# Performance work log

Hardware: AMD Instinct MI355X
Metric: run time of the kernel (lower is better)

## Reference

```python
import jax, jax.numpy as jnp
import numpy as np

EPS = 1e-6
NUM_HEADS = 2
DIM = 64
DIM_OUT = 128
SR = 4
SAMPLE_NUM = 784


def layer_norm(x, g, b, eps=1e-5):
    m = jnp.mean(x, -1, keepdims=True)
    v = jnp.mean((x - m) ** 2, -1, keepdims=True)
    return (x - m) * jax.lax.rsqrt(v + eps) * g + b


def gaussian_filt(x, kernel_size, sigma):
    # depthwise gaussian blur, x: [B, Ch, H, W]
    ch = x.shape[1]
    coord = jnp.arange(kernel_size, dtype=x.dtype)
    xg, yg = jnp.meshgrid(coord, coord, indexing='xy')
    mean = (kernel_size - 1) / 2.0
    var = sigma ** 2.0
    gk = jnp.exp(-((xg - mean) ** 2 + (yg - mean) ** 2) / (2.0 * var)) / (2.0 * np.pi * var)
    gk = gk / jnp.sum(gk)
    kernel = jnp.broadcast_to(gk[None, None], (ch, 1, kernel_size, kernel_size))
    pad = (kernel_size - 1) // 2
    return jax.lax.conv_general_dilated(
        x, kernel, (1, 1), [(pad, pad), (pad, pad)],
        dimension_numbers=('NCHW', 'OIHW', 'NCHW'), feature_group_count=ch)


def reconstruct_feature(feature, mask, kernel_size, sigma):
    if kernel_size <= 1:
        return feature
    feature = feature * mask
    out = gaussian_filt(jnp.concatenate([feature, mask], axis=1), kernel_size, sigma)
    fi = out[:, :-1]
    mi = out[:, -1:]
    fi = fi / (mi + EPS)
    fi = fi * (mi > 0).astype(feature.dtype)
    return feature + (1 - mask) * fi


def token2map(x, loc, H, W, kernel_size, sigma):
    # scatter tokens onto an HxW grid by rounded location, then gaussian-fill holes
    B, N, C = x.shape
    loc = jnp.clip(loc, 0, 1) * jnp.array([W - 1, H - 1], dtype=loc.dtype)
    loc = jnp.round(loc).astype(jnp.int32)
    idx = loc[..., 0] + loc[..., 1] * W + jnp.arange(B, dtype=jnp.int32)[:, None] * (H * W)
    src = jnp.concatenate([x, jnp.ones((B, N, 1), x.dtype)], axis=-1).reshape(B * N, C + 1)
    out = jax.ops.segment_sum(src, idx.reshape(-1), num_segments=B * H * W)
    out = out.reshape(B, H, W, C + 1).transpose(0, 3, 1, 2)
    feat, mask = out[:, :-1], out[:, -1:]
    feat = feat / (mask + EPS)
    mask = (mask > 0).astype(feat.dtype)
    feat = feat * mask
    return reconstruct_feature(feat, mask, kernel_size, sigma)


def grid_sample_bilinear(img, gx, gy):
    # F.grid_sample: bilinear, zeros padding, align_corners=False
    # img: [B, C, H, W]; gx, gy in [-1, 1]: [B, N]
    B, C, H, W = img.shape
    ix = ((gx + 1) * W - 1) / 2
    iy = ((gy + 1) * H - 1) / 2
    x0 = jnp.floor(ix)
    y0 = jnp.floor(iy)
    wx1 = ix - x0
    wy1 = iy - y0
    imgf = img.reshape(B, C, H * W)

    def corner(xc, yc, w):
        valid = (xc >= 0) & (xc < W) & (yc >= 0) & (yc < H)
        xi = jnp.clip(xc, 0, W - 1).astype(jnp.int32)
        yi = jnp.clip(yc, 0, H - 1).astype(jnp.int32)
        lin = (yi * W + xi)[:, None, :]                      # [B,1,N]
        v = jnp.take_along_axis(imgf, lin, axis=2)           # [B,C,N]
        return v * (w * valid)[:, None, :]

    out = (corner(x0, y0, (1 - wx1) * (1 - wy1))
           + corner(x0 + 1, y0, wx1 * (1 - wy1))
           + corner(x0, y0 + 1, (1 - wx1) * wy1)
           + corner(x0 + 1, y0 + 1, wx1 * wy1))
    return out.transpose(0, 2, 1)                            # [B,N,C]


def _forward(x, pos, pos_embed, noise_u, norm_g, norm_b, conf_w, conf_b,
             norm1_g, norm1_b, q_w, k_w, v_w, proj_w, proj_b, sr_w, sr_b,
             srnorm_g, srnorm_b, fc_w, fc_b, norm2_g, norm2_b,
             fc1_w, fc1_b, fc2_w, fc2_b, H, W, N_grid):
    B, N, C = x.shape
    # --- DownLayer: confidence + gumbel top-k over adaptive tokens ---
    conf = layer_norm(x, norm_g, norm_b) @ conf_w + conf_b            # [B,N,1]
    noise = -jnp.log(-jnp.log(noise_u + EPS) + EPS)                   # gumbel noise
    scores = (conf[:, N_grid:] + noise)[..., 0]                       # [B,N-N_grid]
    _, idx = jax.lax.top_k(scores, SAMPLE_NUM)                        # [B,k]
    x_down = jnp.concatenate(
        [x[:, :N_grid], jnp.take_along_axis(x[:, N_grid:], idx[:, :, None], axis=1)], axis=1)
    pos_down = jnp.concatenate(
        [pos[:, :N_grid], jnp.take_along_axis(pos[:, N_grid:], idx[:, :, None], axis=1)], axis=1)

    # --- MyBlock: fc(x) + sr-attention, then MLP (eval mode: dropouts off) ---
    Nd = x_down.shape[1]
    xn = layer_norm(x_down, norm1_g, norm1_b)
    xsn = layer_norm(x, norm1_g, norm1_b)
    q = xn @ q_w                                                      # [B,Nd,DIM_OUT]
    fmap = token2map(xsn, pos, H, W, SR - 1, 2.0)                     # [B,C,H,W]
    xs = jax.lax.conv_general_dilated(
        fmap, sr_w, (SR, SR), 'VALID',
        dimension_numbers=('NCHW', 'OIHW', 'NCHW')) + sr_b[None, :, None, None]
    xs = xs.reshape(B, C, -1).transpose(0, 2, 1)                      # [B,Ns,C]
    xs = layer_norm(xs, srnorm_g, srnorm_b)
    k = xs @ k_w
    v = xs @ v_w
    hd = DIM_OUT // NUM_HEADS
    qh = q.reshape(B, Nd, NUM_HEADS, hd).transpose(0, 2, 1, 3)
    kh = k.reshape(B, -1, NUM_HEADS, hd).transpose(0, 2, 1, 3)
    vh = v.reshape(B, -1, NUM_HEADS, hd).transpose(0, 2, 1, 3)
    scale = (DIM // NUM_HEADS) ** -0.5                                # head_dim from input dim per source
    attn = jax.nn.softmax(jnp.einsum('bhqd,bhkd->bhqk', qh, kh) * scale, axis=-1)
    o = jnp.einsum('bhqk,bhkd->bhqd', attn, vh).transpose(0, 2, 1, 3).reshape(B, Nd, DIM_OUT)
    o = o @ proj_w + proj_b
    x2 = x_down @ fc_w + fc_b + o                                     # use_fc branch (dim_out != dim), alpha=1
    xn2 = layer_norm(x2, norm2_g, norm2_b)
    x2 = x2 + (jax.nn.gelu(xn2 @ fc1_w + fc1_b, approximate=False) @ fc2_w + fc2_b)

    # --- get_pos_embed: bilinear grid_sample of pos_embed at pos_down ---
    Cp = pos_embed.shape[-1]
    pe = jnp.broadcast_to(pos_embed.reshape(1, H, W, Cp).transpose(0, 3, 1, 2), (B, Cp, H, W))
    g = pos_down * 2 - 1
    pos_feat = grid_sample_bilinear(pe, g[..., 0], g[..., 1])         # [B,Nd,Cp]
    return x2 + pos_feat


def setup_inputs() -> dict:
    key = jax.random.key(0)
    ks = jax.random.split(key, 16)
    B, N = 64, 3136
    N_grid = 49

    def w(k, shape, fan):
        return jax.random.normal(k, shape, jnp.float32) / np.sqrt(fan)

    d = {}
    d['x'] = jax.random.normal(ks[0], (B, N, DIM), jnp.float32)
    d['pos'] = jax.random.uniform(ks[1], (B, N, 2), jnp.float32)
    d['pos_embed'] = jax.random.normal(ks[2], (1, N, DIM_OUT), jnp.float32) * 0.02
    d['noise_u'] = jax.random.uniform(ks[3], (B, N - N_grid, 1), jnp.float32)
    d['norm_g'] = jnp.ones(DIM); d['norm_b'] = jnp.zeros(DIM)
    d['conf_w'] = w(ks[4], (DIM, 1), DIM); d['conf_b'] = jnp.zeros(1)
    d['norm1_g'] = jnp.ones(DIM); d['norm1_b'] = jnp.zeros(DIM)
    d['q_w'] = w(ks[5], (DIM, DIM_OUT), DIM)
    d['k_w'] = w(ks[6], (DIM, DIM_OUT), DIM)
    d['v_w'] = w(ks[7], (DIM, DIM_OUT), DIM)
    d['proj_w'] = w(ks[8], (DIM_OUT, DIM_OUT), DIM_OUT); d['proj_b'] = jnp.zeros(DIM_OUT)
    d['sr_w'] = w(ks[9], (DIM, DIM, SR, SR), DIM * SR * SR); d['sr_b'] = jnp.zeros(DIM)
    d['srnorm_g'] = jnp.ones(DIM); d['srnorm_b'] = jnp.zeros(DIM)
    d['fc_w'] = w(ks[10], (DIM, DIM_OUT), DIM); d['fc_b'] = jnp.zeros(DIM_OUT)
    d['norm2_g'] = jnp.ones(DIM_OUT); d['norm2_b'] = jnp.zeros(DIM_OUT)
    d['fc1_w'] = w(ks[11], (DIM_OUT, 4 * DIM_OUT), DIM_OUT); d['fc1_b'] = jnp.zeros(4 * DIM_OUT)
    d['fc2_w'] = w(ks[12], (4 * DIM_OUT, DIM_OUT), 4 * DIM_OUT); d['fc2_b'] = jnp.zeros(DIM_OUT)
    d['H'] = 56; d['W'] = 56; d['N_grid'] = N_grid
    return d


def reference(x, pos, pos_embed, noise_u, norm_g, norm_b, conf_w, conf_b,
              norm1_g, norm1_b, q_w, k_w, v_w, proj_w, proj_b, sr_w, sr_b,
              srnorm_g, srnorm_b, fc_w, fc_b, norm2_g, norm2_b,
              fc1_w, fc1_b, fc2_w, fc2_b, H, W, N_grid):
    return _forward(x, pos, pos_embed, noise_u, norm_g, norm_b, conf_w, conf_b,
                    norm1_g, norm1_b, q_w, k_w, v_w, proj_w, proj_b, sr_w, sr_b,
                    srnorm_g, srnorm_b, fc_w, fc_b, norm2_g, norm2_b,
                    fc1_w, fc1_b, fc2_w, fc2_b, H, W, N_grid)
```

## Files before the change

kernel.cpp:

```cpp
#include <hip/hip_runtime.h>
#include <math.h>

#define DEVINL __device__ __forceinline__

constexpr int B_ = 64;
constexpr int N_ = 3136;
constexpr int C_ = 64;
constexpr int NG = 49;
constexpr int NSAMP = 784;
constexpr int ND = NG + NSAMP;
constexpr int NREST = N_ - NG;
constexpr int H_ = 56, W_ = 56;
constexpr int HW = H_ * W_;
constexpr int BHW = B_ * HW;
constexpr int NS = 14 * 14;
constexpr int KPAD = 224;
constexpr float LN_EPS = 1e-5f;
constexpr float EPS6 = 1e-6f;

typedef __attribute__((ext_vector_type(8))) short short8;
typedef __attribute__((ext_vector_type(4))) float f32x4;

DEVINL unsigned short f2bf(float f) {
  unsigned int u = __float_as_uint(f);
  unsigned int r = u + 0x7FFFu + ((u >> 16) & 1u);
  return (unsigned short)(r >> 16);
}

DEVINL float gelu_fast(float v) {
  float x = v * 0.70710678118654752f;
  float ax = fabsf(x);
  float t = 1.f / fmaf(0.3275911f, ax, 1.f);
  float poly = t * fmaf(t, fmaf(t, fmaf(t, fmaf(t, 1.061405429f, -1.453152027f),
                        1.421413741f), -0.284496736f), 0.254829592f);
  float e = 1.f - poly * __expf(-x * x);
  float erfv = copysignf(e, x);
  return 0.5f * v * (1.f + erfv);
}

__global__ __launch_bounds__(256) void k_conf(
    const float* __restrict__ x, const float* __restrict__ ng, const float* __restrict__ nb,
    const float* __restrict__ cw, const float* __restrict__ cb,
    const float* __restrict__ nu, double* __restrict__ scores) {
  int t = blockIdx.x * 256 + threadIdx.x;
  if (t >= B_ * N_) return;
  int b = t / N_, n = t - b * N_;
  if (n < NG) return;
  const float4* row = (const float4*)(x + (size_t)t * C_);
  float v[C_];
#pragma unroll
  for (int i = 0; i < 16; ++i) {
    float4 r = row[i];
    v[4*i] = r.x; v[4*i+1] = r.y; v[4*i+2] = r.z; v[4*i+3] = r.w;
  }
  double sd = 0.0;
#pragma unroll
  for (int i = 0; i < C_; ++i) sd += (double)v[i];
  double md = sd * (1.0/64.0);
  double vd = 0.0;
#pragma unroll
  for (int i = 0; i < C_; ++i) { double d = (double)v[i] - md; vd += d * d; }
  vd *= (1.0/64.0);
  double rsd = 1.0 / sqrt(vd + 1e-5);
  double conf = (double)cb[0];
#pragma unroll
  for (int i = 0; i < C_; ++i) {
    double xnv = ((double)v[i] - md) * rsd;
    conf += (xnv * (double)ng[i] + (double)nb[i]) * (double)cw[i];
  }
  double u = (double)nu[(size_t)b * NREST + (n - NG)];
  double noise = -log(-log(u + 1e-6) + 1e-6);
  scores[(size_t)b * NREST + (n - NG)] = conf + noise;
}

constexpr int NB = 2048;

__global__ __launch_bounds__(256) void k_topk2(const double* __restrict__ scores,
                                               int* __restrict__ idx) {
  __shared__ double sk[NREST];
  __shared__ int hist[NB];
  __shared__ int bstart[NB];
  __shared__ int fill[NB];
  __shared__ unsigned short order[NREST];
  __shared__ float redmin[256], redmax[256];
  __shared__ int scanbuf[256];
  int b = blockIdx.x, tid = threadIdx.x;
  const double* sc = scores + (size_t)b * NREST;
  float lmin = 3.4e38f, lmax = -3.4e38f;
  for (int i = tid; i < NREST; i += 256) {
    double d = sc[i];
    sk[i] = d;
    float f = (float)d;
    lmin = fminf(lmin, f); lmax = fmaxf(lmax, f);
  }
  for (int i = tid; i < NB; i += 256) hist[i] = 0;
  redmin[tid] = lmin; redmax[tid] = lmax;
  __syncthreads();
  for (int s = 128; s > 0; s >>= 1) {
    if (tid < s) {
      redmin[tid] = fminf(redmin[tid], redmin[tid + s]);
      redmax[tid] = fmaxf(redmax[tid], redmax[tid + s]);
    }
    __syncthreads();
  }
  float fmn = redmin[0];
  float scale = (float)NB / fmaxf(redmax[0] - fmn, 1e-30f);
  for (int i = tid; i < NREST; i += 256) {
    float f = (float)sk[i];
    int bn = (int)((f - fmn) * scale);
    bn = bn < 0 ? 0 : (bn > NB - 1 ? NB - 1 : bn);
    atomicAdd(&hist[bn], 1);
  }
  __syncthreads();
  int base = tid * 8;
  int s_t = 0;
#pragma unroll
  for (int i = 0; i < 8; ++i) s_t += hist[base + i];
  scanbuf[tid] = s_t;
  __syncthreads();
  int val = s_t;
  for (int off = 1; off < 256; off <<= 1) {
    int other = (tid + off < 256) ? scanbuf[tid + off] : 0;
    __syncthreads();
    val += other;
    scanbuf[tid] = val;
    __syncthreads();
  }
  int run = val - s_t;
#pragma unroll
  for (int i = 7; i >= 0; --i) {
    bstart[base + i] = run;
    run += hist[base + i];
  }
  __syncthreads();
  for (int i = tid; i < NB; i += 256) fill[i] = bstart[i];
  __syncthreads();
  for (int i = tid; i < NREST; i += 256) {
    float f = (float)sk[i];
    int bn = (int)((f - fmn) * scale);
    bn = bn < 0 ? 0 : (bn > NB - 1 ? NB - 1 : bn);
    int pos = atomicAdd(&fill[bn], 1);
    order[pos] = (unsigned short)i;
  }
  __syncthreads();
  for (int i = tid; i < NREST; i += 256) {
    double ke = sk[i];
    float f = (float)ke;
    int bn = (int)((f - fmn) * scale);
    bn = bn < 0 ? 0 : (bn > NB - 1 ? NB - 1 : bn);
    int st = bstart[bn], m = hist[bn];
    int r = st;
    for (int p = st; p < st + m; ++p) {
      int j = order[p];
      double kj = sk[j];
      r += (int)((kj > ke) | ((kj == ke) & (j < i)));
    }
    if (r < NSAMP) idx[(size_t)b * NSAMP + r] = i;
  }
}

__global__ __launch_bounds__(256) void k_gather_ln(
    const float* __restrict__ x, const float* __restrict__ pos, const int* __restrict__ idx,
    const float* __restrict__ n1g, const float* __restrict__ n1b,
    float* __restrict__ xd, float* __restrict__ xn, float* __restrict__ pd) {
  int t = blockIdx.x * 256 + threadIdx.x;
  if (t >= B_ * ND) return;
  int b = t / ND, r = t - b * ND;
  int srcn = (r < NG) ? r : (NG + idx[(size_t)b * NSAMP + (r - NG)]);
  const float4* row = (const float4*)(x + ((size_t)b * N_ + srcn) * C_);
  float4* xdr = (float4*)(xd + (size_t)t * C_);
  float v[C_];
  float s = 0.f, ss = 0.f;
#pragma unroll
  for (int i = 0; i < 16; ++i) {
    float4 rr = row[i];
    xdr[i] = rr;
    v[4*i] = rr.x; v[4*i+1] = rr.y; v[4*i+2] = rr.z; v[4*i+3] = rr.w;
    s += rr.x + rr.y + rr.z + rr.w;
    ss += rr.x*rr.x + rr.y*rr.y + rr.z*rr.z + rr.w*rr.w;
  }
  float m = s * (1.f/64.f);
  float var = ss * (1.f/64.f) - m*m;
  float rs = rsqrtf(var + LN_EPS);
#pragma unroll
  for (int i = 0; i < C_; ++i)
    xn[(size_t)t * C_ + i] = (v[i] - m) * rs * n1g[i] + n1b[i];
  pd[(size_t)2*t]   = pos[((size_t)b * N_ + srcn) * 2];
  pd[(size_t)2*t+1] = pos[((size_t)b * N_ + srcn) * 2 + 1];
}

__global__ __launch_bounds__(256) void k_link(
    const float* __restrict__ pos, int* __restrict__ head, int* __restrict__ next) {
  int tok = blockIdx.x * 256 + threadIdx.x;
  if (tok >= B_ * N_) return;
  int b = tok / N_;
  double px = fmin(fmax((double)pos[(size_t)2*tok],   0.0), 1.0) * (double)(W_ - 1);
  double py = fmin(fmax((double)pos[(size_t)2*tok+1], 0.0), 1.0) * (double)(H_ - 1);
  int xi = (int)rint(px), yi = (int)rint(py);
  int p = b * HW + yi * W_ + xi;
  next[tok] = atomicExch(&head[p], tok);
}

__global__ __launch_bounds__(256) void k_accum(
    const float* __restrict__ x, const float* __restrict__ n1g, const float* __restrict__ n1b,
    const int* __restrict__ head, const int* __restrict__ next, float* __restrict__ S) {
  int gt = blockIdx.x * 256 + threadIdx.x;
  int p = gt >> 6, lane = gt & 63;
  if (p >= B_ * HW) return;
  float g = n1g[lane], bb = n1b[lane];
  float acc = 0.f, cnt = 0.f;
  int tok = head[p];
  while (tok >= 0) {
    float v = x[(size_t)tok * C_ + lane];
    float s = v, ss = v * v;
#pragma unroll
    for (int m = 32; m > 0; m >>= 1) {
      s += __shfl_xor(s, m);
      ss += __shfl_xor(ss, m);
    }
    float mean = s * (1.f/64.f);
    float var = ss * (1.f/64.f) - mean * mean;
    float rs = rsqrtf(var + LN_EPS);
    acc += (v - mean) * rs * g + bb;
    cnt += 1.f;
    tok = next[tok];
  }
  float* base = S + (size_t)p * 65;
  base[lane] = acc;
  if (lane == 0) base[64] = cnt;
}

__global__ __launch_bounds__(256) void k_transpose(const float* __restrict__ S,
                                                   float* __restrict__ T,
                                                   float* __restrict__ M) {
  __shared__ float ls[64 * 65];
  int g0 = blockIdx.x * 64;
  int b = g0 / HW, p0 = g0 - b * HW;
  const float4* src = (const float4*)(S + (size_t)g0 * 65);
  for (int i = threadIdx.x; i < (64 * 65) / 4; i += 256)
    *(float4*)&ls[i * 4] = src[i];
  __syncthreads();
  for (int i = threadIdx.x; i < 64 * 64; i += 256) {
    int c = i >> 6, px = i & 63;
    T[((size_t)(b * 64 + c)) * HW + p0 + px] = ls[px * 65 + c];
  }
  for (int i = threadIdx.x; i < 64; i += 256)
    M[(size_t)g0 + i] = ls[i * 65 + 64];
}

__global__ __launch_bounds__(256) void k_coef(const float* __restrict__ M, float* __restrict__ Kc) {
  int t = blockIdx.x * 256 + threadIdx.x;
  if (t >= BHW) return;
  int b = t / HW, p = t - b * HW;
  int y = p / W_, x = p - y * W_;
  const float* Mb = M + (size_t)b * HW;
  const float e1 = 0.882496902584595f;
  const float e2 = 0.778800783071405f;
  const float Z = 1.f + 4.f * (e1 + e2);
  float m0 = Mb[p];
  float mb0 = m0 > 0.f ? 1.f : 0.f;
  float cfac = mb0 / (m0 + EPS6);
  float sc[9];
  float mi = 0.f;
  int q = 0;
#pragma unroll
  for (int dy = -1; dy <= 1; ++dy) {
#pragma unroll
    for (int dx = -1; dx <= 1; ++dx) {
      int ny = y + dy, nx = x + dx;
      bool in = (ny >= 0 && ny < H_ && nx >= 0 && nx < W_);
      float w = ((dx == 0 && dy == 0) ? 1.f : ((dx*dx + dy*dy) == 1 ? e1 : e2)) / Z;
      float mm = in ? Mb[ny * W_ + nx] : 0.f;
      float mb = mm > 0.f ? 1.f : 0.f;
      mi += w * mb;
      sc[q] = in ? (w * mb / (mm + EPS6)) : 0.f;
      ++q;
    }
  }
  float outer = (1.f - mb0) * ((mi > 0.f ? 1.f : 0.f) / (mi + EPS6));
#pragma unroll
  for (int qq = 0; qq < 9; ++qq) {
    float cq = outer * sc[qq];
    if (qq == 4) cq += cfac;
    Kc[(size_t)qq * BHW + t] = cq;
  }
}

__global__ __launch_bounds__(256) void k_filter2(
    const float* __restrict__ T, const float* __restrict__ Kc, float* __restrict__ P) {
  int plane = blockIdx.x;
  int b = plane >> 6, c = plane & 63;
  int tid = threadIdx.x;
  const float* Tp = T + (size_t)plane * HW;
  const float* Kb = Kc + (size_t)b * HW;
  for (int p0 = 0; p0 < HW; p0 += 256) {
    int p = p0 + tid;
    if (p < HW) {
      int y = p / W_, x = p - y * W_;
      float acc = 0.f;
      int q = 0;
#pragma unroll
      for (int dy = -1; dy <= 1; ++dy) {
#pragma unroll
        for (int dx = -1; dx <= 1; ++dx) {
          int ny = y + dy; ny = ny < 0 ? 0 : (ny > H_ - 1 ? H_ - 1 : ny);
          int nx = x + dx; nx = nx < 0 ? 0 : (nx > W_ - 1 ? W_ - 1 : nx);
          acc += Kb[(size_t)q * BHW + p] * Tp[ny * W_ + nx];
          ++q;
        }
      }
      int j = (y >> 2) * 14 + (x >> 2);
      int colb = ((y & 3) << 2) + (x & 3);
      P[((size_t)(b * NS + j)) * 1024 + c * 16 + colb] = acc;
    }
  }
}

__global__ __launch_bounds__(256) void k_wtp(const float* __restrict__ srw,
                                             unsigned short* __restrict__ Wcp) {
  int t = blockIdx.x * 256 + threadIdx.x;
  if (t >= 65536) return;
  int j = t & 7;
  int n = (t >> 3) & 63;
  int s = (t >> 9) & 15;
  int ch = t >> 13;
  int k = ch * 128 + (s >> 2) * 32 + (s & 3) * 8 + j;
  int ci = k >> 4, r = k & 15;
  Wcp[t] = f2bf(srw[(((size_t)n * 64 + ci) << 4) + r]);
}

__global__ __launch_bounds__(256) void k_wpack(const float* __restrict__ W1, const float* __restrict__ W2,
    unsigned short* __restrict__ W1q, unsigned short* __restrict__ W2q) {
  int t = blockIdx.x * 256 + threadIdx.x;
  if (t >= 65536) return;
  {
    int j = t & 7;
    int nl = (t >> 3) & 63;
    int s = (t >> 9) & 15;
    int hh = t >> 13;
    int k = (s >> 2) * 32 + (s & 3) * 8 + j;
    int n = hh * 64 + nl;
    W1q[t] = f2bf(W1[(size_t)k * 512 + n]);
  }
  {
    int j = t & 7;
    int n = (t >> 3) & 127;
    int s = (t >> 10) & 7;
    int hh = t >> 13;
    int k = hh * 64 + (s >> 2) * 32 + (s & 3) * 8 + j;
    W2q[t] = f2bf(W2[(size_t)k * 128 + n]);
  }
}

__global__ __launch_bounds__(256) void k_conv(
    const float* __restrict__ P, const unsigned short* __restrict__ Wcp,
    const float* __restrict__ bias, float* __restrict__ out) {
  __shared__ __align__(16) unsigned short sA[64 * 128];
  __shared__ __align__(16) unsigned short sW[8192];
  int bm = blockIdx.x * 64;
  int tid = threadIdx.x;
  int wv = tid >> 6, lane = tid & 63, quad = lane >> 4, l16 = lane & 15;

  const short8* gw = (const short8*)Wcp;
  short8* dw = (short8*)sW;

  short8 rw[4];
  float4 fa[4][2];
#pragma unroll
  for (int i = 0; i < 4; ++i) rw[i] = gw[i * 256 + tid];
#pragma unroll
  for (int i = 0; i < 4; ++i) {
    int u = i * 256 + tid;
    int row = u >> 4, ck = u & 15;
    const float* src = P + (size_t)(bm + row) * 1024 + ck * 8;
    fa[i][0] = *(const float4*)src;
    fa[i][1] = *(const float4*)(src + 4);
  }

  f32x4 acc[4];
#pragma unroll
  for (int ct = 0; ct < 4; ++ct) acc[ct] = (f32x4){0.f, 0.f, 0.f, 0.f};

  for (int ch = 0; ch < 8; ++ch) {
#pragma unroll
    for (int i = 0; i < 4; ++i) {
      dw[i * 256 + tid] = rw[i];
      int u = i * 256 + tid;
      int row = u >> 4, ck = u & 15;
      short8 p;
      p[0]=(short)f2bf(fa[i][0].x); p[1]=(short)f2bf(fa[i][0].y);
      p[2]=(short)f2bf(fa[i][0].z); p[3]=(short)f2bf(fa[i][0].w);
      p[4]=(short)f2bf(fa[i][1].x); p[5]=(short)f2bf(fa[i][1].y);
      p[6]=(short)f2bf(fa[i][1].z); p[7]=(short)f2bf(fa[i][1].w);
      *(short8*)&sA[row * 128 + (((ck ^ row) & 15) << 3)] = p;
    }
    __syncthreads();
    if (ch < 7) {
      int wbase = (ch + 1) * 1024;
#pragma unroll
      for (int i = 0; i < 4; ++i) rw[i] = gw[wbase + i * 256 + tid];
#pragma unroll
      for (int i = 0; i < 4; ++i) {
        int u = i * 256 + tid;
        int row = u >> 4, ck = u & 15;
        const float* src = P + (size_t)(bm + row) * 1024 + (ch + 1) * 128 + ck * 8;
        fa[i][0] = *(const float4*)src;
        fa[i][1] = *(const float4*)(src + 4);
      }
    }
#pragma unroll
    for (int kc = 0; kc < 4; ++kc) {
      int row = wv * 16 + l16;
      int ck = kc * 4 + quad;
      short8 af = *(const short8*)&sA[row * 128 + (((ck ^ row) & 15) << 3)];
      int s = kc * 4 + quad;
#pragma unroll
      for (int ct = 0; ct < 4; ++ct) {
        short8 bf = *(const short8*)&sW[(s * 64 + ct * 16 + l16) << 3];
        acc[ct] = __builtin_amdgcn_mfma_f32_16x16x32_bf16(af, bf, acc[ct], 0, 0, 0);
      }
    }
    __syncthreads();
  }
#pragma unroll
  for (int ct = 0; ct < 4; ++ct)
#pragma unroll
    for (int r = 0; r < 4; ++r) {
      int row = bm + wv * 16 + quad * 4 + r;
      int col = ct * 16 + l16;
      out[(size_t)row * 64 + col] = acc[ct][r] + bias[col];
    }
}

__global__ __launch_bounds__(256) void k_gemm(
    const float* __restrict__ A, const float* __restrict__ Bw,
    const float* __restrict__ bias, const float* __restrict__ add,
    float* __restrict__ Cout, int M, int N, int K) {
  __shared__ float sA[16][68];
  __shared__ float sB[16][64];
  int bm = blockIdx.x * 64, bn = blockIdx.y * 64;
  int tid = threadIdx.x;
  int tx = tid & 15, ty = tid >> 4;
  float acc[4][4] = {{0.f}};
  for (int k0 = 0; k0 < K; k0 += 16) {
    int e = tid << 2;
    int am = e >> 4, ak = e & 15;
    float4 a4 = *(const float4*)(A + (size_t)(bm + am) * K + k0 + ak);
    sA[ak + 0][am] = a4.x; sA[ak + 1][am] = a4.y; sA[ak + 2][am] = a4.z; sA[ak + 3][am] = a4.w;
    int bk = e >> 6, nn = e & 63;
    float4 b4 = *(const float4*)(Bw + (size_t)(k0 + bk) * N + bn + nn);
    *(float4*)&sB[bk][nn] = b4;
    __syncthreads();
#pragma unroll
    for (int kk = 0; kk < 16; ++kk) {
      float a[4], bb[4];
#pragma unroll
      for (int i = 0; i < 4; ++i) a[i] = sA[kk][ty * 4 + i];
#pragma unroll
      for (int i = 0; i < 4; ++i) bb[i] = sB[kk][tx * 4 + i];
#pragma unroll
      for (int i = 0; i < 4; ++i)
#pragma unroll
        for (int jj = 0; jj < 4; ++jj) acc[i][jj] += a[i] * bb[jj];
    }
    __syncthreads();
  }
#pragma unroll
  for (int i = 0; i < 4; ++i) {
    int row = bm + ty * 4 + i;
#pragma unroll
    for (int jj = 0; jj < 4; ++jj) {
      int col = bn + tx * 4 + jj;
      float v = acc[i][jj];
      if (bias) v += bias[col];
      if (add) v += add[(size_t)row * N + col];
      Cout[(size_t)row * N + col] = v;
    }
  }
}

__global__ __launch_bounds__(256) void k_mlp(
    const float* __restrict__ A, const unsigned short* __restrict__ W1q, const float* __restrict__ b1,
    const unsigned short* __restrict__ W2q, const float* __restrict__ b2, float* __restrict__ out) {
  __shared__ __align__(16) unsigned short sA[64 * 128];
  __shared__ __align__(16) unsigned short sW1[8192];
  __shared__ __align__(16) unsigned short sW2[8192];
  __shared__ __align__(16) unsigned short sH[4][16 * 64];
  int bm = blockIdx.x * 64;
  int tid = threadIdx.x;
  int wv = tid >> 6, lane = tid & 63, quad = lane >> 4, l16 = lane & 15;

  const short8* g1 = (const short8*)W1q;
  const short8* g2 = (const short8*)W2q;
  short8* d1 = (short8*)sW1;
  short8* d2 = (short8*)sW2;

  short8 r1[4], r2[4];
#pragma unroll
  for (int i = 0; i < 4; ++i) {
    r1[i] = g1[i * 256 + tid];
    r2[i] = g2[i * 256 + tid];
  }

  for (int t = tid; t < 64 * 16; t += 256) {
    int row = t >> 4, ck = t & 15;
    const float* src = A + (size_t)(bm + row) * 128 + ck * 8;
    float4 a = *(const float4*)src;
    float4 c = *(const float4*)(src + 4);
    short8 p;
    p[0]=(short)f2bf(a.x); p[1]=(short)f2bf(a.y); p[2]=(short)f2bf(a.z); p[3]=(short)f2bf(a.w);
    p[4]=(short)f2bf(c.x); p[5]=(short)f2bf(c.y); p[6]=(short)f2bf(c.z); p[7]=(short)f2bf(c.w);
    *(short8*)&sA[row * 128 + (((ck ^ row) & 15) << 3)] = p;
  }
  __syncthreads();

  f32x4 oacc[8];
#pragma unroll
  for (int ct = 0; ct < 8; ++ct) oacc[ct] = (f32x4){0.f, 0.f, 0.f, 0.f};

  for (int hh = 0; hh < 8; ++hh) {
#pragma unroll
    for (int i = 0; i < 4; ++i) {
      d1[i * 256 + tid] = r1[i];
      d2[i * 256 + tid] = r2[i];
    }
    __syncthreads();
    if (hh < 7) {
      int base = (hh + 1) * 1024;
#pragma unroll
      for (int i = 0; i < 4; ++i) {
        r1[i] = g1[base + i * 256 + tid];
        r2[i] = g2[base + i * 256 + tid];
      }
    }
    f32x4 acc1[4];
#pragma unroll
    for (int ct = 0; ct < 4; ++ct) acc1[ct] = (f32x4){0.f, 0.f, 0.f, 0.f};
#pragma unroll
    for (int kc = 0; kc < 4; ++kc) {
      int row = wv * 16 + l16;
      int ck = kc * 4 + quad;
      short8 af = *(const short8*)&sA[row * 128 + (((ck ^ row) & 15) << 3)];
      int s = kc * 4 + quad;
#pragma unroll
      for (int ct = 0; ct < 4; ++ct) {
        short8 bf = *(const short8*)&sW1[(s * 64 + ct * 16 + l16) << 3];
        acc1[ct] = __builtin_amdgcn_mfma_f32_16x16x32_bf16(af, bf, acc1[ct], 0, 0, 0);
      }
    }
#pragma unroll
    for (int ct = 0; ct < 4; ++ct)
#pragma unroll
      for (int r = 0; r < 4; ++r) {
        float v = acc1[ct][r] + b1[hh * 64 + ct * 16 + l16];
        v = gelu_fast(v);
        int rit = quad * 4 + r;
        int col = ct * 16 + l16;
        int ck = (col >> 3) ^ (rit & 7);
        sH[wv][rit * 64 + ((ck & 7) << 3) + (col & 7)] = f2bf(v);
      }
#pragma unroll
    for (int kg = 0; kg < 2; ++kg) {
      int ckh = kg * 4 + quad;
      short8 hf = *(const short8*)&sH[wv][l16 * 64 + (((ckh ^ (l16 & 7)) & 7) << 3)];
      int s = kg * 4 + quad;
#pragma unroll
      for (int ct = 0; ct < 8; ++ct) {
        short8 bf = *(const short8*)&sW2[(s * 128 + ct * 16 + l16) << 3];
        oacc[ct] = __builtin_amdgcn_mfma_f32_16x16x32_bf16(hf, bf, oacc[ct], 0, 0, 0);
      }
    }
    __syncthreads();
  }
#pragma unroll
  for (int ct = 0; ct < 8; ++ct)
#pragma unroll
    for (int r = 0; r < 4; ++r) {
      int row = bm + wv * 16 + quad * 4 + r;
      int col = ct * 16 + l16;
      out[(size_t)row * 128 + col] += oacc[ct][r] + b2[col];
    }
}

__global__ __launch_bounds__(256) void k_ln128(const float* __restrict__ in, const float* __restrict__ g,
    const float* __restrict__ bb, float* __restrict__ out, int rows) {
  int t = blockIdx.x * 256 + threadIdx.x;
  if (t >= rows) return;
  const float4* row = (const float4*)(in + (size_t)t * 128);
  float4 v[32];
  float s = 0.f, ss = 0.f;
#pragma unroll
  for (int i = 0; i < 32; ++i) {
    float4 r = row[i]; v[i] = r;
    s += r.x + r.y + r.z + r.w;
    ss += r.x*r.x + r.y*r.y + r.z*r.z + r.w*r.w;
  }
  float m = s * (1.f/128.f);
  float var = ss * (1.f/128.f) - m*m;
  float rs = rsqrtf(var + LN_EPS);
  float4* orow = (float4*)(out + (size_t)t * 128);
#pragma unroll
  for (int i = 0; i < 32; ++i) {
    float4 r = v[i];
    float4 o;
    o.x = (r.x - m) * rs * g[4*i+0] + bb[4*i+0];
    o.y = (r.y - m) * rs * g[4*i+1] + bb[4*i+1];
    o.z = (r.z - m) * rs * g[4*i+2] + bb[4*i+2];
    o.w = (r.w - m) * rs * g[4*i+3] + bb[4*i+3];
    orow[i] = o;
  }
}

__global__ __launch_bounds__(256) void k_ln64(const float* __restrict__ in, const float* __restrict__ g,
    const float* __restrict__ bb, float* __restrict__ out, int rows) {
  int t = blockIdx.x * 256 + threadIdx.x;
  if (t >= rows) return;
  const float4* row = (const float4*)(in + (size_t)t * 64);
  float v[64];
  float s = 0.f, ss = 0.f;
#pragma unroll
  for (int i = 0; i < 16; ++i) {
    float4 r = row[i];
    v[4*i] = r.x; v[4*i+1] = r.y; v[4*i+2] = r.z; v[4*i+3] = r.w;
    s += r.x + r.y + r.z + r.w;
    ss += r.x*r.x + r.y*r.y + r.z*r.z + r.w*r.w;
  }
  float m = s * (1.f/64.f);
  float var = ss * (1.f/64.f) - m*m;
  float rs = rsqrtf(var + LN_EPS);
#pragma unroll
  for (int i = 0; i < 64; ++i)
    out[(size_t)t * 64 + i] = (v[i] - m) * rs * g[i] + bb[i];
}

__global__ __launch_bounds__(256) void k_attn(const float* __restrict__ q,
    const float* __restrict__ kg, const float* __restrict__ vg, float* __restrict__ o) {
  __shared__ __align__(16) unsigned short ldsKP[14848];
  __shared__ __align__(16) unsigned short ldsV[16128];
  int blk = blockIdx.x;
  int chunk = blk % 14;
  int bh = blk / 14;
  int h = bh & 1, b = bh >> 1;
  int tid = threadIdx.x;
  int wv = tid >> 6, lane = tid & 63;
  int quad = lane >> 4, l16 = lane & 15;

  const float* kb = kg + (size_t)b * NS * 128 + h * 64;
  const float* vb = vg + (size_t)b * NS * 128 + h * 64;

  for (int t = tid; t < KPAD * 8; t += 256) {
    int key = t >> 3, ck = t & 7;
    short8 pk, pv;
    if (key < NS) {
      const float* ksrc = kb + (size_t)key * 128 + ck * 8;
      const float* vsrc = vb + (size_t)key * 128 + ck * 8;
      float4 a = *(const float4*)ksrc;
      float4 c = *(const float4*)(ksrc + 4);
      pk[0]=(short)f2bf(a.x); pk[1]=(short)f2bf(a.y); pk[2]=(short)f2bf(a.z); pk[3]=(short)f2bf(a.w);
      pk[4]=(short)f2bf(c.x); pk[5]=(short)f2bf(c.y); pk[6]=(short)f2bf(c.z); pk[7]=(short)f2bf(c.w);
      float4 e = *(const float4*)vsrc;
      float4 g = *(const float4*)(vsrc + 4);
      pv[0]=(short)f2bf(e.x); pv[1]=(short)f2bf(e.y); pv[2]=(short)f2bf(e.z); pv[3]=(short)f2bf(e.w);
      pv[4]=(short)f2bf(g.x); pv[5]=(short)f2bf(g.y); pv[6]=(short)f2bf(g.z); pv[7]=(short)f2bf(g.w);
    } else {
      pk = (short8)0; pv = (short8)0;
    }
    *(short8*)&ldsKP[key * 64 + ((ck ^ (key & 7)) << 3)] = pk;
    *(short8*)&ldsV[key * 72 + ck * 8] = pv;
  }

  int qrow = chunk * 64 + wv * 16 + l16;
  int qrowc = qrow < ND ? qrow : ND - 1;
  const float* qsrc = q + ((size_t)b * ND + qrowc) * 128 + h * 64 + quad * 8;
  short8 aq0, aq1;
  {
    float4 a = *(const float4*)qsrc;
    float4 c = *(const float4*)(qsrc + 4);
    aq0[0]=(short)f2bf(a.x); aq0[1]=(short)f2bf(a.y); aq0[2]=(short)f2bf(a.z); aq0[3]=(short)f2bf(a.w);
    aq0[4]=(short)f2bf(c.x); aq0[5]=(short)f2bf(c.y); aq0[6]=(short)f2bf(c.z); aq0[7]=(short)f2bf(c.w);
    float4 e = *(const float4*)(qsrc + 32);
    float4 g = *(const float4*)(qsrc + 36);
    aq1[0]=(short)f2bf(e.x); aq1[1]=(short)f2bf(e.y); aq1[2]=(short)f2bf(e.z); aq1[3]=(short)f2bf(e.w);
    aq1[4]=(short)f2bf(g.x); aq1[5]=(short)f2bf(g.y); aq1[6]=(short)f2bf(g.z); aq1[7]=(short)f2bf(g.w);
  }
  __syncthreads();

  f32x4 acc[14];
#pragma unroll
  for (int ct = 0; ct < 14; ++ct) {
    int key = ct * 16 + l16;
    short8 bk0 = *(const short8*)&ldsKP[key * 64 + ((quad ^ (key & 7)) << 3)];
    short8 bk1 = *(const short8*)&ldsKP[key * 64 + (((4 + quad) ^ (key & 7)) << 3)];
    f32x4 z = {0.f, 0.f, 0.f, 0.f};
    z = __builtin_amdgcn_mfma_f32_16x16x32_bf16(aq0, bk0, z, 0, 0, 0);
    z = __builtin_amdgcn_mfma_f32_16x16x32_bf16(aq1, bk1, z, 0, 0, 0);
    acc[ct] = z;
  }

  const float scale = 0.17677669529663687f;
  float rmax[4] = {-1e30f, -1e30f, -1e30f, -1e30f};
#pragma unroll
  for (int ct = 0; ct < 14; ++ct) {
    bool msk = (ct * 16 + l16) >= NS;
#pragma unroll
    for (int r = 0; r < 4; ++r) {
      float sv = msk ? -1e30f : acc[ct][r] * scale;
      acc[ct][r] = sv;
      rmax[r] = fmaxf(rmax[r], sv);
    }
  }
#pragma unroll
  for (int m = 1; m < 16; m <<= 1)
#pragma unroll
    for (int r = 0; r < 4; ++r) rmax[r] = fmaxf(rmax[r], __shfl_xor(rmax[r], m));
  float rsum[4] = {0.f, 0.f, 0.f, 0.f};
#pragma unroll
  for (int ct = 0; ct < 14; ++ct)
#pragma unroll
    for (int r = 0; r < 4; ++r) {
      float e = __expf(acc[ct][r] - rmax[r]);
      acc[ct][r] = e;
      rsum[r] += e;
    }
#pragma unroll
  for (int m = 1; m < 16; m <<= 1)
#pragma unroll
    for (int r = 0; r < 4; ++r) rsum[r] += __shfl_xor(rsum[r], m);
  float rinv[4];
#pragma unroll
  for (int r = 0; r < 4; ++r) rinv[r] = 1.f / rsum[r];

  __syncthreads();

#pragma unroll
  for (int ct = 0; ct < 14; ++ct)
#pragma unroll
    for (int r = 0; r < 4; ++r) {
      int prow = wv * 16 + quad * 4 + r;
      ldsKP[prow * 232 + ct * 16 + l16] = f2bf(acc[ct][r] * rinv[r]);
    }
  __syncthreads();

  f32x4 oacc[4];
#pragma unroll
  for (int ot = 0; ot < 4; ++ot) oacc[ot] = (f32x4){0.f, 0.f, 0.f, 0.f};
#pragma unroll
  for (int kc = 0; kc < 7; ++kc) {
    short8 ap = *(const short8*)&ldsKP[(wv * 16 + l16) * 232 + kc * 32 + quad * 8];
    int keybase = kc * 32 + quad * 8;
#pragma unroll
    for (int ot = 0; ot < 4; ++ot) {
      int dcol = ot * 16 + l16;
      short8 bv;
#pragma unroll
      for (int j = 0; j < 8; ++j) bv[j] = (short)ldsV[(keybase + j) * 72 + dcol];
      oacc[ot] = __builtin_amdgcn_mfma_f32_16x16x32_bf16(ap, bv, oacc[ot], 0, 0, 0);
    }
  }

#pragma unroll
  for (int ot = 0; ot < 4; ++ot)
#pragma unroll
    for (int r = 0; r < 4; ++r) {
      int rowg = chunk * 64 + wv * 16 + quad * 4 + r;
      if (rowg < ND)
        o[((size_t)b * ND + rowg) * 128 + h * 64 + ot * 16 + l16] = oacc[ot][r];
    }
}

__global__ __launch_bounds__(256) void k_posfeat(const float* __restrict__ pd,
    const float* __restrict__ pe, float* __restrict__ out) {
  int t = blockIdx.x * 256 + threadIdx.x;
  int row = t >> 5, lane = t & 31;
  if (row >= B_ * ND) return;
  float gx = pd[(size_t)2*row] * 2.f - 1.f;
  float gy = pd[(size_t)2*row+1] * 2.f - 1.f;
  float ix = ((gx + 1.f) * 56.f - 1.f) * 0.5f;
  float iy = ((gy + 1.f) * 56.f - 1.f) * 0.5f;
  float x0 = floorf(ix), y0 = floorf(iy);
  float wx1 = ix - x0, wy1 = iy - y0;
  float wx0 = 1.f - wx1, wy0 = 1.f - wy1;
  float4 acc = make_float4(0.f, 0.f, 0.f, 0.f);
#pragma unroll
  for (int cy = 0; cy < 2; ++cy) {
#pragma unroll
    for (int cx = 0; cx < 2; ++cx) {
      float xc = x0 + (float)cx, yc = y0 + (float)cy;
      float wgt = (cx ? wx1 : wx0) * (cy ? wy1 : wy0);
      bool valid = (xc >= 0.f) && (xc < 56.f) && (yc >= 0.f) && (yc < 56.f);
      if (valid) {
        int lin = (int)yc * 56 + (int)xc;
        float4 pv = ((const float4*)(pe + (size_t)lin * 128))[lane];
        acc.x += wgt * pv.x; acc.y += wgt * pv.y;
        acc.z += wgt * pv.z; acc.w += wgt * pv.w;
      }
    }
  }
  float4* op = (float4*)(out + (size_t)row * 128) + lane;
  float4 cur = *op;
  cur.x += acc.x; cur.y += acc.y; cur.z += acc.z; cur.w += acc.w;
  *op = cur;
}

extern "C" void kernel_launch(void* const* d_in, const int* in_sizes, int n_in,
                              void* d_out, int out_size, void* d_ws, size_t ws_size,
                              hipStream_t stream) {
  const float* x      = (const float*)d_in[0];
  const float* pos    = (const float*)d_in[1];
  const float* pe     = (const float*)d_in[2];
  const float* nu     = (const float*)d_in[3];
  const float* norm_g = (const float*)d_in[4];
  const float* norm_b = (const float*)d_in[5];
  const float* conf_w = (const float*)d_in[6];
  const float* conf_b = (const float*)d_in[7];
  const float* n1g    = (const float*)d_in[8];
  const float* n1b    = (const float*)d_in[9];
  const float* q_w    = (const float*)d_in[10];
  const float* k_w    = (const float*)d_in[11];
  const float* v_w    = (const float*)d_in[12];
  const float* proj_w = (const float*)d_in[13];
  const float* proj_b = (const float*)d_in[14];
  const float* sr_w   = (const float*)d_in[15];
  const float* sr_b   = (const float*)d_in[16];
  const float* srn_g  = (const float*)d_in[17];
  const float* srn_b  = (const float*)d_in[18];
  const float* fc_w   = (const float*)d_in[19];
  const float* fc_b   = (const float*)d_in[20];
  const float* n2g    = (const float*)d_in[21];
  const float* n2b    = (const float*)d_in[22];
  const float* fc1_w  = (const float*)d_in[23];
  const float* fc1_b  = (const float*)d_in[24];
  const float* fc2_w  = (const float*)d_in[25];
  const float* fc2_b  = (const float*)d_in[26];

  char* ws = (char*)d_ws;
  double*         scores = (double*)(ws + 0);
  int*            idx    = (int*)(ws + 1605632);
  float*          xd     = (float*)(ws + 1835008);
  float*          xn     = (float*)(ws + 15728640);
  float*          pd     = (float*)(ws + 29491200);
  float*          qb     = (float*)(ws + 30408704);
  float*          ob     = (float*)(ws + 58720256);
  unsigned short* Wcp    = (unsigned short*)(ws + 86507520);
  unsigned short* W1p    = (unsigned short*)(ws + 86769664);
  unsigned short* W2p    = (unsigned short*)(ws + 86900736);
  char*           big    = ws + 87031808;
  float*          S      = (float*)big;
  float*          T      = qb;
  float*          Kc     = (float*)(big + 52183040);
  float*          P      = (float*)big;
  float*          xs_c   = (float*)(big + 59408384);
  float*          xs_n   = (float*)(big + 62619648);
  float*          kbuf   = (float*)(big + 65830912);
  float*          vbuf   = (float*)(big + 72253440);
  float*          Mbuf   = (float*)(big + 78675968);
  int*            head   = (int*)(big + 79478784);
  int*            nxt    = (int*)(big + 80281600);
  float*          O2     = qb;
  float*          xn2    = ob;
  float*          out    = (float*)d_out;

  k_conf<<<(B_ * N_) / 256, 256, 0, stream>>>(x, norm_g, norm_b, conf_w, conf_b, nu, scores);
  k_topk2<<<B_, 256, 0, stream>>>(scores, idx);
  k_gather_ln<<<(B_ * ND + 255) / 256, 256, 0, stream>>>(x, pos, idx, n1g, n1b, xd, xn, pd);
  hipMemsetAsync(head, 0xFF, (size_t)B_ * HW * sizeof(int), stream);
  k_link<<<(B_ * N_ + 255) / 256, 256, 0, stream>>>(pos, head, nxt);
  k_accum<<<(B_ * HW * 64) / 256, 256, 0, stream>>>(x, n1g, n1b, head, nxt, S);
  k_transpose<<<BHW / 64, 256, 0, stream>>>(S, T, Mbuf);
  k_coef<<<BHW / 256, 256, 0, stream>>>(Mbuf, Kc);
  k_filter2<<<B_ * 64, 256, 0, stream>>>(T, Kc, P);
  k_wtp<<<65536 / 256, 256, 0, stream>>>(sr_w, Wcp);
  k_wpack<<<65536 / 256, 256, 0, stream>>>(fc1_w, fc2_w, W1p, W2p);
  k_conv<<<B_ * NS / 64, 256, 0, stream>>>(P, Wcp, sr_b, xs_c);
  k_ln64<<<(B_ * NS + 255) / 256, 256, 0, stream>>>(xs_c, srn_g, srn_b, xs_n, B_ * NS);
  dim3 g_kv(B_ * NS / 64, 2);
  k_gemm<<<g_kv, 256, 0, stream>>>(xs_n, k_w, nullptr, nullptr, kbuf, B_ * NS, 128, 64);
  k_gemm<<<g_kv, 256, 0, stream>>>(xs_n, v_w, nullptr, nullptr, vbuf, B_ * NS, 128, 64);
  dim3 g_row(B_ * ND / 64, 2);
  k_gemm<<<g_row, 256, 0, stream>>>(xn, q_w, nullptr, nullptr, qb, B_ * ND, 128, 64);
  k_attn<<<B_ * 2 * 14, 256, 0, stream>>>(qb, kbuf, vbuf, ob);
  k_gemm<<<g_row, 256, 0, stream>>>(ob, proj_w, proj_b, nullptr, O2, B_ * ND, 128, 128);
  k_gemm<<<g_row, 256, 0, stream>>>(xd, fc_w, fc_b, O2, out, B_ * ND, 128, 64);
  k_ln128<<<(B_ * ND + 255) / 256, 256, 0, stream>>>(out, n2g, n2b, xn2, B_ * ND);
  k_mlp<<<B_ * ND / 64, 256, 0, stream>>>(xn2, W1p, fc1_b, W2p, fc2_b, out);
  k_posfeat<<<(B_ * ND * 32) / 256, 256, 0, stream>>>(pd, pe, out);
}
```

Measured before the change: 575.1 us.

## Fuse layernorms into conv and MLP GEMM kernels

The separate k_ln64 and k_ln128 kernels are removed. The sr-norm layernorm now runs in the k_conv epilogue, using wave shuffles to reduce each row across its 64 output columns. The norm2 layernorm now runs in the k_mlp prologue, with each lane holding its row's A fragments in registers instead of staging them through LDS. This saves two launches and a full write and re-read of the intermediate activations, at the cost of more registers per thread and a one-pass variance formula.

```diff
diff --git a/kernel.cpp b/kernel.cpp
--- a/kernel.cpp
+++ b/kernel.cpp
@@ -354,7 +354,8 @@
 
 __global__ __launch_bounds__(256) void k_conv(
     const float* __restrict__ P, const unsigned short* __restrict__ Wcp,
-    const float* __restrict__ bias, float* __restrict__ out) {
+    const float* __restrict__ bias, const float* __restrict__ sg,
+    const float* __restrict__ sb, float* __restrict__ xsn) {
   __shared__ __align__(16) unsigned short sA[64 * 128];
   __shared__ __align__(16) unsigned short sW[8192];
   int bm = blockIdx.x * 64;
@@ -422,13 +423,40 @@
     }
     __syncthreads();
   }
+  float vv[4][4];
+  float rsum[4], rss[4];
+#pragma unroll
+  for (int r = 0; r < 4; ++r) { rsum[r] = 0.f; rss[r] = 0.f; }
+#pragma unroll
+  for (int ct = 0; ct < 4; ++ct)
+#pragma unroll
+    for (int r = 0; r < 4; ++r) {
+      float v = acc[ct][r] + bias[ct * 16 + l16];
+      vv[ct][r] = v;
+      rsum[r] += v;
+      rss[r] += v * v;
+    }
+#pragma unroll
+  for (int m = 1; m < 16; m <<= 1)
+#pragma unroll
+    for (int r = 0; r < 4; ++r) {
+      rsum[r] += __shfl_xor(rsum[r], m);
+      rss[r]  += __shfl_xor(rss[r], m);
+    }
+  float mean[4], rsl[4];
+#pragma unroll
+  for (int r = 0; r < 4; ++r) {
+    mean[r] = rsum[r] * (1.f/64.f);
+    float var = rss[r] * (1.f/64.f) - mean[r] * mean[r];
+    rsl[r] = rsqrtf(var + LN_EPS);
+  }
 #pragma unroll
   for (int ct = 0; ct < 4; ++ct)
 #pragma unroll
     for (int r = 0; r < 4; ++r) {
       int row = bm + wv * 16 + quad * 4 + r;
       int col = ct * 16 + l16;
-      out[(size_t)row * 64 + col] = acc[ct][r] + bias[col];
+      xsn[(size_t)row * 64 + col] = (vv[ct][r] - mean[r]) * rsl[r] * sg[col] + sb[col];
     }
 }
 
@@ -480,9 +508,10 @@
 }
 
 __global__ __launch_bounds__(256) void k_mlp(
-    const float* __restrict__ A, const unsigned short* __restrict__ W1q, const float* __restrict__ b1,
-    const unsigned short* __restrict__ W2q, const float* __restrict__ b2, float* __restrict__ out) {
-  __shared__ __align__(16) unsigned short sA[64 * 128];
+    const float* __restrict__ A, const float* __restrict__ gg, const float* __restrict__ gb,
+    const unsigned short* __restrict__ W1q, const float* __restrict__ b1,
+    const unsigned short* __restrict__ W2q, const float* __restrict__ b2,
+    float* __restrict__ out) {
   __shared__ __align__(16) unsigned short sW1[8192];
   __shared__ __align__(16) unsigned short sW2[8192];
   __shared__ __align__(16) unsigned short sH[4][16 * 64];
@@ -502,17 +531,41 @@
     r2[i] = g2[i * 256 + tid];
   }
 
-  for (int t = tid; t < 64 * 16; t += 256) {
-    int row = t >> 4, ck = t & 15;
-    const float* src = A + (size_t)(bm + row) * 128 + ck * 8;
-    float4 a = *(const float4*)src;
-    float4 c = *(const float4*)(src + 4);
-    short8 p;
-    p[0]=(short)f2bf(a.x); p[1]=(short)f2bf(a.y); p[2]=(short)f2bf(a.z); p[3]=(short)f2bf(a.w);
-    p[4]=(short)f2bf(c.x); p[5]=(short)f2bf(c.y); p[6]=(short)f2bf(c.z); p[7]=(short)f2bf(c.w);
-    *(short8*)&sA[row * 128 + (((ck ^ row) & 15) << 3)] = p;
-  }
-  __syncthreads();
+  int row = bm + wv * 16 + l16;
+  const float* arow = A + (size_t)row * 128 + quad * 8;
+  float av[4][8];
+  float s = 0.f, ss = 0.f;
+#pragma unroll
+  for (int kc = 0; kc < 4; ++kc) {
+    float4 a = *(const float4*)(arow + kc * 32);
+    float4 c = *(const float4*)(arow + kc * 32 + 4);
+    av[kc][0]=a.x; av[kc][1]=a.y; av[kc][2]=a.z; av[kc][3]=a.w;
+    av[kc][4]=c.x; av[kc][5]=c.y; av[kc][6]=c.z; av[kc][7]=c.w;
+    s += a.x+a.y+a.z+a.w + c.x+c.y+c.z+c.w;
+    ss += a.x*a.x+a.y*a.y+a.z*a.z+a.w*a.w + c.x*c.x+c.y*c.y+c.z*c.z+c.w*c.w;
+  }
+  s += __shfl_xor(s, 16);  ss += __shfl_xor(ss, 16);
+  s += __shfl_xor(s, 32);  ss += __shfl_xor(ss, 32);
+  float m = s * (1.f/128.f);
+  float var = ss * (1.f/128.f) - m * m;
+  float rs = rsqrtf(var + LN_EPS);
+  short8 af[4];
+#pragma unroll
+  for (int kc = 0; kc < 4; ++kc) {
+    int c0 = kc * 32 + quad * 8;
+    float4 ga = *(const float4*)(gg + c0);
+    float4 gc = *(const float4*)(gg + c0 + 4);
+    float4 ba = *(const float4*)(gb + c0);
+    float4 bc = *(const float4*)(gb + c0 + 4);
+    af[kc][0] = (short)f2bf((av[kc][0]-m)*rs*ga.x + ba.x);
+    af[kc][1] = (short)f2bf((av[kc][1]-m)*rs*ga.y + ba.y);
+    af[kc][2] = (short)f2bf((av[kc][2]-m)*rs*ga.z + ba.z);
+    af[kc][3] = (short)f2bf((av[kc][3]-m)*rs*ga.w + ba.w);
+    af[kc][4] = (short)f2bf((av[kc][4]-m)*rs*gc.x + bc.x);
+    af[kc][5] = (short)f2bf((av[kc][5]-m)*rs*gc.y + bc.y);
+    af[kc][6] = (short)f2bf((av[kc][6]-m)*rs*gc.z + bc.z);
+    af[kc][7] = (short)f2bf((av[kc][7]-m)*rs*gc.w + bc.w);
+  }
 
   f32x4 oacc[8];
 #pragma unroll
@@ -538,14 +591,11 @@
     for (int ct = 0; ct < 4; ++ct) acc1[ct] = (f32x4){0.f, 0.f, 0.f, 0.f};
 #pragma unroll
     for (int kc = 0; kc < 4; ++kc) {
-      int row = wv * 16 + l16;
-      int ck = kc * 4 + quad;
-      short8 af = *(const short8*)&sA[row * 128 + (((ck ^ row) & 15) << 3)];
-      int s = kc * 4 + quad;
+      int sidx = kc * 4 + quad;
 #pragma unroll
       for (int ct = 0; ct < 4; ++ct) {
-        short8 bf = *(const short8*)&sW1[(s * 64 + ct * 16 + l16) << 3];
-        acc1[ct] = __builtin_amdgcn_mfma_f32_16x16x32_bf16(af, bf, acc1[ct], 0, 0, 0);
+        short8 bf = *(const short8*)&sW1[(sidx * 64 + ct * 16 + l16) << 3];
+        acc1[ct] = __builtin_amdgcn_mfma_f32_16x16x32_bf16(af[kc], bf, acc1[ct], 0, 0, 0);
       }
     }
 #pragma unroll
@@ -563,10 +613,10 @@
     for (int kg = 0; kg < 2; ++kg) {
       int ckh = kg * 4 + quad;
       short8 hf = *(const short8*)&sH[wv][l16 * 64 + (((ckh ^ (l16 & 7)) & 7) << 3)];
-      int s = kg * 4 + quad;
+      int sidx = kg * 4 + quad;
 #pragma unroll
       for (int ct = 0; ct < 8; ++ct) {
-        short8 bf = *(const short8*)&sW2[(s * 128 + ct * 16 + l16) << 3];
+        short8 bf = *(const short8*)&sW2[(sidx * 128 + ct * 16 + l16) << 3];
         oacc[ct] = __builtin_amdgcn_mfma_f32_16x16x32_bf16(hf, bf, oacc[ct], 0, 0, 0);
       }
     }
@@ -576,61 +626,10 @@
   for (int ct = 0; ct < 8; ++ct)
 #pragma unroll
     for (int r = 0; r < 4; ++r) {
-      int row = bm + wv * 16 + quad * 4 + r;
+      int orow = bm + wv * 16 + quad * 4 + r;
       int col = ct * 16 + l16;
-      out[(size_t)row * 128 + col] += oacc[ct][r] + b2[col];
-    }
-}
-
-__global__ __launch_bounds__(256) void k_ln128(const float* __restrict__ in, const float* __restrict__ g,
-    const float* __restrict__ bb, float* __restrict__ out, int rows) {
-  int t = blockIdx.x * 256 + threadIdx.x;
-  if (t >= rows) return;
-  const float4* row = (const float4*)(in + (size_t)t * 128);
-  float4 v[32];
-  float s = 0.f, ss = 0.f;
-#pragma unroll
-  for (int i = 0; i < 32; ++i) {
-    float4 r = row[i]; v[i] = r;
-    s += r.x + r.y + r.z + r.w;
-    ss += r.x*r.x + r.y*r.y + r.z*r.z + r.w*r.w;
-  }
-  float m = s * (1.f/128.f);
-  float var = ss * (1.f/128.f) - m*m;
-  float rs = rsqrtf(var + LN_EPS);
-  float4* orow = (float4*)(out + (size_t)t * 128);
-#pragma unroll
-  for (int i = 0; i < 32; ++i) {
-    float4 r = v[i];
-    float4 o;
-    o.x = (r.x - m) * rs * g[4*i+0] + bb[4*i+0];
-    o.y = (r.y - m) * rs * g[4*i+1] + bb[4*i+1];
-    o.z = (r.z - m) * rs * g[4*i+2] + bb[4*i+2];
-    o.w = (r.w - m) * rs * g[4*i+3] + bb[4*i+3];
-    orow[i] = o;
-  }
-}
-
-__global__ __launch_bounds__(256) void k_ln64(const float* __restrict__ in, const float* __restrict__ g,
-    const float* __restrict__ bb, float* __restrict__ out, int rows) {
-  int t = blockIdx.x * 256 + threadIdx.x;
-  if (t >= rows) return;
-  const float4* row = (const float4*)(in + (size_t)t * 64);
-  float v[64];
-  float s = 0.f, ss = 0.f;
-#pragma unroll
-  for (int i = 0; i < 16; ++i) {
-    float4 r = row[i];
-    v[4*i] = r.x; v[4*i+1] = r.y; v[4*i+2] = r.z; v[4*i+3] = r.w;
-    s += r.x + r.y + r.z + r.w;
-    ss += r.x*r.x + r.y*r.y + r.z*r.z + r.w*r.w;
-  }
-  float m = s * (1.f/64.f);
-  float var = ss * (1.f/64.f) - m*m;
-  float rs = rsqrtf(var + LN_EPS);
-#pragma unroll
-  for (int i = 0; i < 64; ++i)
-    out[(size_t)t * 64 + i] = (v[i] - m) * rs * g[i] + bb[i];
+      out[(size_t)orow * 128 + col] += oacc[ct][r] + b2[col];
+    }
 }
 
 __global__ __launch_bounds__(256) void k_attn(const float* __restrict__ q,
@@ -849,7 +848,6 @@
   float*          T      = qb;
   float*          Kc     = (float*)(big + 52183040);
   float*          P      = (float*)big;
-  float*          xs_c   = (float*)(big + 59408384);
   float*          xs_n   = (float*)(big + 62619648);
   float*          kbuf   = (float*)(big + 65830912);
   float*          vbuf   = (float*)(big + 72253440);
@@ -857,7 +855,6 @@
   int*            head   = (int*)(big + 79478784);
   int*            nxt    = (int*)(big + 80281600);
   float*          O2     = qb;
-  float*          xn2    = ob;
   float*          out    = (float*)d_out;
 
   k_conf<<<(B_ * N_) / 256, 256, 0, stream>>>(x, norm_g, norm_b, conf_w, conf_b, nu, scores);
@@ -871,8 +868,7 @@
   k_filter2<<<B_ * 64, 256, 0, stream>>>(T, Kc, P);
   k_wtp<<<65536 / 256, 256, 0, stream>>>(sr_w, Wcp);
   k_wpack<<<65536 / 256, 256, 0, stream>>>(fc1_w, fc2_w, W1p, W2p);
-  k_conv<<<B_ * NS / 64, 256, 0, stream>>>(P, Wcp, sr_b, xs_c);
-  k_ln64<<<(B_ * NS + 255) / 256, 256, 0, stream>>>(xs_c, srn_g, srn_b, xs_n, B_ * NS);
+  k_conv<<<B_ * NS / 64, 256, 0, stream>>>(P, Wcp, sr_b, srn_g, srn_b, xs_n);
   dim3 g_kv(B_ * NS / 64, 2);
   k_gemm<<<g_kv, 256, 0, stream>>>(xs_n, k_w, nullptr, nullptr, kbuf, B_ * NS, 128, 64);
   k_gemm<<<g_kv, 256, 0, stream>>>(xs_n, v_w, nullptr, nullptr, vbuf, B_ * NS, 128, 64);
@@ -881,7 +877,6 @@
   k_attn<<<B_ * 2 * 14, 256, 0, stream>>>(qb, kbuf, vbuf, ob);
   k_gemm<<<g_row, 256, 0, stream>>>(ob, proj_w, proj_b, nullptr, O2, B_ * ND, 128, 128);
   k_gemm<<<g_row, 256, 0, stream>>>(xd, fc_w, fc_b, O2, out, B_ * ND, 128, 64);
-  k_ln128<<<(B_ * ND + 255) / 256, 256, 0, stream>>>(out, n2g, n2b, xn2, B_ * ND);
-  k_mlp<<<B_ * ND / 64, 256, 0, stream>>>(xn2, W1p, fc1_b, W2p, fc2_b, out);
+  k_mlp<<<B_ * ND / 64, 256, 0, stream>>>(out, n2g, n2b, W1p, fc1_b, W2p, fc2_b, out);
   k_posfeat<<<(B_ * ND * 32) / 256, 256, 0, stream>>>(pd, pe, out);
 }
```

Measured after the change: 570.8 us. No clear change (-0.8%).
